# Optimization experiments

Measured on AMD Instinct MI355X. Metric: run time of the kernel, lower is better.

Reference implementation:

```python
import jax, jax.numpy as jnp
import numpy as np

KNN = 16


def _knn_idx(k, ref_xyz, query_xyz):
    # squared euclidean distances: (B, Nq, Nr)
    q2 = jnp.sum(query_xyz * query_xyz, axis=-1, keepdims=True)        # (B, Nq, 1)
    r2 = jnp.sum(ref_xyz * ref_xyz, axis=-1)[:, None, :]               # (B, 1, Nr)
    cross = jnp.einsum('bqc,brc->bqr', query_xyz, ref_xyz)             # (B, Nq, Nr)
    dist = q2 + r2 - 2.0 * cross
    neg_vals, idx = jax.lax.top_k(-dist, k)                            # k smallest dists
    return -neg_vals, idx


def setup_inputs() -> dict:
    key = jax.random.key(0)
    k1, k2, k3, k4 = jax.random.split(key, 4)
    B, N_prev, N_cur, C = 1, 8192, 4096, 256
    return {
        'xyz_prev': jax.random.normal(k1, (B, N_prev, 3), dtype=jnp.float32),
        'xyz_cur': jax.random.normal(k2, (B, N_cur, 3), dtype=jnp.float32),
        'feat_prev': jax.random.normal(k3, (B, N_prev, C), dtype=jnp.float32),
        'feat_cur': jax.random.normal(k4, (B, N_cur, C), dtype=jnp.float32),
    }


def reference(xyz_prev, xyz_cur, feat_prev, feat_cur):
    k = KNN
    _, idx = _knn_idx(k, xyz_prev, xyz_cur)                 # (B, Nq, k) per-batch-local indices
    B, Nq, _ = idx.shape
    C = feat_prev.shape[-1]
    idx_flat = idx.reshape(-1, k).astype(jnp.int32)          # (B*Nq, k)
    prev_flat = feat_prev.reshape(-1, C)                     # (B*Nprev, C)
    cur_flat = feat_cur.reshape(-1, C)                       # (B*Nq, C)
    # faithful to original: gather from flattened table with local indices (batch_dims=0)
    prev_sel = prev_flat[idx_flat]                           # (B*Nq, k, C)
    cur_sel = jnp.broadcast_to(cur_flat[:, None, :], (B * Nq, k, C))
    inter = jnp.concatenate([prev_sel - cur_sel, cur_sel], axis=-1)  # (B*Nq, k, 2C)
    return inter.reshape(B, Nq * k, 2 * C)
```

## Files before the change

kernel.cpp:

```cpp
#include <hip/hip_runtime.h>
#include <stdint.h>

#define KNN 16

typedef float vfloat4 __attribute__((ext_vector_type(4)));

__device__ __forceinline__ uint32_t fkey(float f) {
    uint32_t u = __float_as_uint(f);
    return (u & 0x80000000u) ? ~u : (u | 0x80000000u);
}

__device__ __forceinline__ float inv_fkey_hi(unsigned long long key) {
    const uint32_t k = (uint32_t)(key >> 32);
    if (k == 0xFFFFFFFFu) return __builtin_inff();
    const uint32_t u = (k & 0x80000000u) ? (k ^ 0x80000000u) : ~k;
    return __uint_as_float(u);
}

__device__ __forceinline__ unsigned long long bcast64(unsigned long long x, int l) {
    const uint32_t lo = (uint32_t)__builtin_amdgcn_readlane((int)(uint32_t)x, l);
    const uint32_t hi = (uint32_t)__builtin_amdgcn_readlane((int)(uint32_t)(x >> 32), l);
    return ((unsigned long long)hi << 32) | lo;
}

__device__ __forceinline__ unsigned long long shup1_64(unsigned long long x) {
    const uint32_t lo = (uint32_t)__builtin_amdgcn_update_dpp(
        0, (int)(uint32_t)x, 0x111, 0xF, 0xF, true);
    const uint32_t hi = (uint32_t)__builtin_amdgcn_update_dpp(
        0, (int)(uint32_t)(x >> 32), 0x111, 0xF, 0xF, true);
    return ((unsigned long long)hi << 32) | lo;
}

__global__ __launch_bounds__(256) void prep_kernel(
    const float* __restrict__ xyz_prev, vfloat4* __restrict__ P, int n_prev)
{
    const int i = blockIdx.x * 256 + threadIdx.x;
    if (i >= n_prev) return;
    const float x = xyz_prev[3 * i + 0];
    const float y = xyz_prev[3 * i + 1];
    const float z = xyz_prev[3 * i + 2];
    const float r2 = __fadd_rn(__fadd_rn(__fmul_rn(x, x), __fmul_rn(y, y)),
                               __fmul_rn(z, z));
    vfloat4 v = {x, y, z, r2};
    P[i] = v;
}

__global__ __launch_bounds__(256, 8) void knn_kernel(
    const vfloat4* __restrict__ P, const float* __restrict__ xyz_cur,
    int* __restrict__ knn_idx, int n_prev, int n_cur)
{
    __shared__ unsigned long long smem[2][2][KNN];
    const int lane = threadIdx.x & 63;
    const int qq   = threadIdx.x >> 7;
    const int h    = (threadIdx.x >> 6) & 1;
    const int q    = blockIdx.x * 2 + qq;
    const bool active = q < n_cur;

    if (active) {
        const float qx = xyz_cur[3 * q + 0];
        const float qy = xyz_cur[3 * q + 1];
        const float qz = xyz_cur[3 * q + 2];
        const float q2 = __fadd_rn(__fadd_rn(__fmul_rn(qx, qx), __fmul_rn(qy, qy)),
                                   __fmul_rn(qz, qz));

        const int half_len = ((n_prev + 127) >> 7) << 6;
        const int base = h * half_len;
        const int end  = min((h + 1) * half_len, n_prev);
        const int cnt  = (end > base) ? (end - base) : 0;

        unsigned long long v;
        {
            const int r = base + lane;
            const vfloat4 p = P[r < n_prev ? r : 0];
            const float cr = __fmaf_rn(p.z, qz, __fmaf_rn(p.y, qy, __fmul_rn(p.x, qx)));
            const float dist = __fsub_rn(__fadd_rn(q2, p.w), __fmul_rn(2.0f, cr));
            v = (r < end)
                ? (((unsigned long long)fkey(dist) << 32) | (uint32_t)r)
                : ~0ull;
        }
#pragma unroll
        for (int k = 2; k <= 64; k <<= 1) {
#pragma unroll
            for (int j = k >> 1; j > 0; j >>= 1) {
                const unsigned long long o = __shfl_xor(v, j, 64);
                const bool keepMin = (((lane & k) == 0) == ((lane & j) == 0));
                const bool omin = o < v;
                v = (keepMin == omin) ? o : v;
            }
        }
        unsigned long long lkey = (lane < KNN) ? v : ~0ull;
        unsigned long long tau = bcast64(lkey, 15);
        float tauf = inv_fkey_hi(tau);

        const int n_full = cnt >> 6;
        int t = 1;
        for (; t + 3 < n_full; t += 4) {
            vfloat4 pv[4];
#pragma unroll
            for (int u = 0; u < 4; ++u)
                pv[u] = P[base + ((t + u) << 6) + lane];
#pragma unroll
            for (int u = 0; u < 4; ++u) {
                const int rbase = base + ((t + u) << 6);
                const vfloat4 p = pv[u];
                const float cr = __fmaf_rn(p.z, qz, __fmaf_rn(p.y, qy, __fmul_rn(p.x, qx)));
                const float dist = __fsub_rn(__fadd_rn(q2, p.w), __fmul_rn(2.0f, cr));
                unsigned long long mask = __ballot(dist < tauf);
                while (mask) {
                    const int b = (int)__builtin_ctzll(mask);
                    mask &= mask - 1;
                    const float bd = __uint_as_float(
                        (uint32_t)__builtin_amdgcn_readlane((int)__float_as_uint(dist), b));
                    const unsigned long long bk =
                        (((unsigned long long)fkey(bd)) << 32) | (uint32_t)(rbase + b);
                    if (bk < tau) {
                        const unsigned long long sh = shup1_64(lkey);
                        unsigned long long nk;
                        if (lkey < bk) nk = lkey;
                        else nk = (lane == 0 || sh < bk) ? bk : sh;
                        tau = bcast64(nk, 15);
                        tauf = inv_fkey_hi(tau);
                        if (lane < KNN) lkey = nk;
                    }
                }
            }
        }
        for (; t < n_full; ++t) {
            const int rbase = base + (t << 6);
            const vfloat4 p = P[rbase + lane];
            const float cr = __fmaf_rn(p.z, qz, __fmaf_rn(p.y, qy, __fmul_rn(p.x, qx)));
            const float dist = __fsub_rn(__fadd_rn(q2, p.w), __fmul_rn(2.0f, cr));
            unsigned long long mask = __ballot(dist < tauf);
            while (mask) {
                const int b = (int)__builtin_ctzll(mask);
                mask &= mask - 1;
                const float bd = __uint_as_float(
                    (uint32_t)__builtin_amdgcn_readlane((int)__float_as_uint(dist), b));
                const unsigned long long bk =
                    (((unsigned long long)fkey(bd)) << 32) | (uint32_t)(rbase + b);
                if (bk < tau) {
                    const unsigned long long sh = shup1_64(lkey);
                    unsigned long long nk;
                    if (lkey < bk) nk = lkey;
                    else nk = (lane == 0 || sh < bk) ? bk : sh;
                    tau = bcast64(nk, 15);
                    tauf = inv_fkey_hi(tau);
                    if (lane < KNN) lkey = nk;
                }
            }
        }
        if (n_full >= 1 && (cnt & 63)) {
            const int rbase = base + (n_full << 6);
            const int r = rbase + lane;
            const vfloat4 p = P[r < n_prev ? r : 0];
            const float cr = __fmaf_rn(p.z, qz, __fmaf_rn(p.y, qy, __fmul_rn(p.x, qx)));
            float dist = __fsub_rn(__fadd_rn(q2, p.w), __fmul_rn(2.0f, cr));
            if (r >= end) dist = __builtin_inff();
            unsigned long long mask = __ballot(dist < tauf);
            while (mask) {
                const int b = (int)__builtin_ctzll(mask);
                mask &= mask - 1;
                const float bd = __uint_as_float(
                    (uint32_t)__builtin_amdgcn_readlane((int)__float_as_uint(dist), b));
                const unsigned long long bk =
                    (((unsigned long long)fkey(bd)) << 32) | (uint32_t)(rbase + b);
                if (bk < tau) {
                    const unsigned long long sh = shup1_64(lkey);
                    unsigned long long nk;
                    if (lkey < bk) nk = lkey;
                    else nk = (lane == 0 || sh < bk) ? bk : sh;
                    tau = bcast64(nk, 15);
                    tauf = inv_fkey_hi(tau);
                    if (lane < KNN) lkey = nk;
                }
            }
        }

        if (lane < KNN) smem[qq][h][lane] = lkey;
    }

    __syncthreads();

    if (active && h == 0) {
        unsigned long long v = ~0ull;
        if (lane < 16)      v = smem[qq][0][lane];
        else if (lane < 32) v = smem[qq][1][31 - lane];
#pragma unroll
        for (int j = 16; j > 0; j >>= 1) {
            const unsigned long long o = __shfl_xor(v, j, 64);
            const bool keepMin = ((lane & j) == 0);
            const bool omin = o < v;
            v = (keepMin == omin) ? o : v;
        }
        if (lane < KNN)
            knn_idx[q * KNN + lane] = (int)(v & 0xffffffffu);
    }
}

__global__ __launch_bounds__(256) void combine_kernel(
    const float* __restrict__ feat_prev, const float* __restrict__ feat_cur,
    const int* __restrict__ knn_idx, float* __restrict__ out,
    int n_cur, int c4)
{
    const int w = blockIdx.x * 4 + (threadIdx.x >> 6);
    const int lane = threadIdx.x & 63;
    const int q = w >> 2;
    const int jg = (w & 3) * 4;
    if (q >= n_cur) return;

    int nb[4];
#pragma unroll
    for (int j = 0; j < 4; ++j)
        nb[j] = knn_idx[q * KNN + jg + j];

    const vfloat4* pbase = (const vfloat4*)feat_prev;
    const vfloat4* crow  = (const vfloat4*)feat_cur + (size_t)q * c4;
    const int c8 = 2 * c4;

    for (int i = lane; i < c4; i += 64) {
        const vfloat4 c = crow[i];
        vfloat4 p[4];
#pragma unroll
        for (int j = 0; j < 4; ++j)
            p[j] = pbase[(size_t)nb[j] * c4 + i];

#pragma unroll
        for (int j = 0; j < 4; ++j) {
            vfloat4* orow = (vfloat4*)out + (size_t)(q * KNN + jg + j) * c8;
            __builtin_nontemporal_store(p[j] - c, orow + i);
            __builtin_nontemporal_store(c, orow + c4 + i);
        }
    }
}

extern "C" void kernel_launch(void* const* d_in, const int* in_sizes, int n_in,
                              void* d_out, int out_size, void* d_ws, size_t ws_size,
                              hipStream_t stream) {
    const float* xyz_prev  = (const float*)d_in[0];
    const float* xyz_cur   = (const float*)d_in[1];
    const float* feat_prev = (const float*)d_in[2];
    const float* feat_cur  = (const float*)d_in[3];
    float* out = (float*)d_out;

    const int n_prev = in_sizes[0] / 3;
    const int n_cur  = in_sizes[1] / 3;
    const int C      = in_sizes[2] / n_prev;

    vfloat4* P = (vfloat4*)d_ws;
    int* knn = (int*)((char*)d_ws + (size_t)n_prev * sizeof(vfloat4));

    prep_kernel<<<(n_prev + 255) / 256, 256, 0, stream>>>(xyz_prev, P, n_prev);

    const int knn_blocks = (n_cur + 1) / 2;
    knn_kernel<<<knn_blocks, 256, 0, stream>>>(P, xyz_cur, knn, n_prev, n_cur);

    const int n_waves = n_cur * 4;
    combine_kernel<<<(n_waves + 3) / 4, 256, 0, stream>>>(feat_prev, feat_cur,
                                                          knn, out, n_cur, C / 4);
}
```

Baseline: 206.3 us.

## Assign one wave per KNN query instead of splitting across two waves

```diff
diff --git a/kernel.cpp b/kernel.cpp
--- a/kernel.cpp
+++ b/kernel.cpp
@@ -49,85 +49,51 @@
     const vfloat4* __restrict__ P, const float* __restrict__ xyz_cur,
     int* __restrict__ knn_idx, int n_prev, int n_cur)
 {
-    __shared__ unsigned long long smem[2][2][KNN];
     const int lane = threadIdx.x & 63;
-    const int qq   = threadIdx.x >> 7;
-    const int h    = (threadIdx.x >> 6) & 1;
-    const int q    = blockIdx.x * 2 + qq;
-    const bool active = q < n_cur;
-
-    if (active) {
-        const float qx = xyz_cur[3 * q + 0];
-        const float qy = xyz_cur[3 * q + 1];
-        const float qz = xyz_cur[3 * q + 2];
-        const float q2 = __fadd_rn(__fadd_rn(__fmul_rn(qx, qx), __fmul_rn(qy, qy)),
-                                   __fmul_rn(qz, qz));
-
-        const int half_len = ((n_prev + 127) >> 7) << 6;
-        const int base = h * half_len;
-        const int end  = min((h + 1) * half_len, n_prev);
-        const int cnt  = (end > base) ? (end - base) : 0;
-
-        unsigned long long v;
-        {
-            const int r = base + lane;
-            const vfloat4 p = P[r < n_prev ? r : 0];
-            const float cr = __fmaf_rn(p.z, qz, __fmaf_rn(p.y, qy, __fmul_rn(p.x, qx)));
-            const float dist = __fsub_rn(__fadd_rn(q2, p.w), __fmul_rn(2.0f, cr));
-            v = (r < end)
-                ? (((unsigned long long)fkey(dist) << 32) | (uint32_t)r)
-                : ~0ull;
-        }
-#pragma unroll
-        for (int k = 2; k <= 64; k <<= 1) {
-#pragma unroll
-            for (int j = k >> 1; j > 0; j >>= 1) {
-                const unsigned long long o = __shfl_xor(v, j, 64);
-                const bool keepMin = (((lane & k) == 0) == ((lane & j) == 0));
-                const bool omin = o < v;
-                v = (keepMin == omin) ? o : v;
-            }
-        }
-        unsigned long long lkey = (lane < KNN) ? v : ~0ull;
-        unsigned long long tau = bcast64(lkey, 15);
-        float tauf = inv_fkey_hi(tau);
-
-        const int n_full = cnt >> 6;
-        int t = 1;
-        for (; t + 3 < n_full; t += 4) {
-            vfloat4 pv[4];
-#pragma unroll
-            for (int u = 0; u < 4; ++u)
-                pv[u] = P[base + ((t + u) << 6) + lane];
-#pragma unroll
-            for (int u = 0; u < 4; ++u) {
-                const int rbase = base + ((t + u) << 6);
-                const vfloat4 p = pv[u];
-                const float cr = __fmaf_rn(p.z, qz, __fmaf_rn(p.y, qy, __fmul_rn(p.x, qx)));
-                const float dist = __fsub_rn(__fadd_rn(q2, p.w), __fmul_rn(2.0f, cr));
-                unsigned long long mask = __ballot(dist < tauf);
-                while (mask) {
-                    const int b = (int)__builtin_ctzll(mask);
-                    mask &= mask - 1;
-                    const float bd = __uint_as_float(
-                        (uint32_t)__builtin_amdgcn_readlane((int)__float_as_uint(dist), b));
-                    const unsigned long long bk =
-                        (((unsigned long long)fkey(bd)) << 32) | (uint32_t)(rbase + b);
-                    if (bk < tau) {
-                        const unsigned long long sh = shup1_64(lkey);
-                        unsigned long long nk;
-                        if (lkey < bk) nk = lkey;
-                        else nk = (lane == 0 || sh < bk) ? bk : sh;
-                        tau = bcast64(nk, 15);
-                        tauf = inv_fkey_hi(tau);
-                        if (lane < KNN) lkey = nk;
-                    }
-                }
-            }
-        }
-        for (; t < n_full; ++t) {
-            const int rbase = base + (t << 6);
-            const vfloat4 p = P[rbase + lane];
+    const int q = blockIdx.x * 4 + (threadIdx.x >> 6);
+    if (q >= n_cur) return;
+
+    const float qx = xyz_cur[3 * q + 0];
+    const float qy = xyz_cur[3 * q + 1];
+    const float qz = xyz_cur[3 * q + 2];
+    const float q2 = __fadd_rn(__fadd_rn(__fmul_rn(qx, qx), __fmul_rn(qy, qy)),
+                               __fmul_rn(qz, qz));
+
+    unsigned long long v;
+    {
+        const int r = lane;
+        const vfloat4 p = P[r < n_prev ? r : 0];
+        const float cr = __fmaf_rn(p.z, qz, __fmaf_rn(p.y, qy, __fmul_rn(p.x, qx)));
+        const float dist = __fsub_rn(__fadd_rn(q2, p.w), __fmul_rn(2.0f, cr));
+        v = (r < n_prev)
+            ? (((unsigned long long)fkey(dist) << 32) | (uint32_t)r)
+            : ~0ull;
+    }
+#pragma unroll
+    for (int k = 2; k <= 64; k <<= 1) {
+#pragma unroll
+        for (int j = k >> 1; j > 0; j >>= 1) {
+            const unsigned long long o = __shfl_xor(v, j, 64);
+            const bool keepMin = (((lane & k) == 0) == ((lane & j) == 0));
+            const bool omin = o < v;
+            v = (keepMin == omin) ? o : v;
+        }
+    }
+    unsigned long long lkey = (lane < KNN) ? v : ~0ull;
+    unsigned long long tau = bcast64(lkey, 15);
+    float tauf = inv_fkey_hi(tau);
+
+    const int n_full = n_prev >> 6;
+    int t = 1;
+    for (; t + 3 < n_full; t += 4) {
+        vfloat4 pv[4];
+#pragma unroll
+        for (int u = 0; u < 4; ++u)
+            pv[u] = P[((t + u) << 6) + lane];
+#pragma unroll
+        for (int u = 0; u < 4; ++u) {
+            const int rbase = (t + u) << 6;
+            const vfloat4 p = pv[u];
             const float cr = __fmaf_rn(p.z, qz, __fmaf_rn(p.y, qy, __fmul_rn(p.x, qx)));
             const float dist = __fsub_rn(__fadd_rn(q2, p.w), __fmul_rn(2.0f, cr));
             unsigned long long mask = __ballot(dist < tauf);
@@ -149,52 +115,60 @@
                 }
             }
         }
-        if (n_full >= 1 && (cnt & 63)) {
-            const int rbase = base + (n_full << 6);
-            const int r = rbase + lane;
-            const vfloat4 p = P[r < n_prev ? r : 0];
-            const float cr = __fmaf_rn(p.z, qz, __fmaf_rn(p.y, qy, __fmul_rn(p.x, qx)));
-            float dist = __fsub_rn(__fadd_rn(q2, p.w), __fmul_rn(2.0f, cr));
-            if (r >= end) dist = __builtin_inff();
-            unsigned long long mask = __ballot(dist < tauf);
-            while (mask) {
-                const int b = (int)__builtin_ctzll(mask);
-                mask &= mask - 1;
-                const float bd = __uint_as_float(
-                    (uint32_t)__builtin_amdgcn_readlane((int)__float_as_uint(dist), b));
-                const unsigned long long bk =
-                    (((unsigned long long)fkey(bd)) << 32) | (uint32_t)(rbase + b);
-                if (bk < tau) {
-                    const unsigned long long sh = shup1_64(lkey);
-                    unsigned long long nk;
-                    if (lkey < bk) nk = lkey;
-                    else nk = (lane == 0 || sh < bk) ? bk : sh;
-                    tau = bcast64(nk, 15);
-                    tauf = inv_fkey_hi(tau);
-                    if (lane < KNN) lkey = nk;
-                }
+    }
+    for (; t < n_full; ++t) {
+        const int rbase = t << 6;
+        const vfloat4 p = P[rbase + lane];
+        const float cr = __fmaf_rn(p.z, qz, __fmaf_rn(p.y, qy, __fmul_rn(p.x, qx)));
+        const float dist = __fsub_rn(__fadd_rn(q2, p.w), __fmul_rn(2.0f, cr));
+        unsigned long long mask = __ballot(dist < tauf);
+        while (mask) {
+            const int b = (int)__builtin_ctzll(mask);
+            mask &= mask - 1;
+            const float bd = __uint_as_float(
+                (uint32_t)__builtin_amdgcn_readlane((int)__float_as_uint(dist), b));
+            const unsigned long long bk =
+                (((unsigned long long)fkey(bd)) << 32) | (uint32_t)(rbase + b);
+            if (bk < tau) {
+                const unsigned long long sh = shup1_64(lkey);
+                unsigned long long nk;
+                if (lkey < bk) nk = lkey;
+                else nk = (lane == 0 || sh < bk) ? bk : sh;
+                tau = bcast64(nk, 15);
+                tauf = inv_fkey_hi(tau);
+                if (lane < KNN) lkey = nk;
             }
         }
-
-        if (lane < KNN) smem[qq][h][lane] = lkey;
-    }
-
-    __syncthreads();
-
-    if (active && h == 0) {
-        unsigned long long v = ~0ull;
-        if (lane < 16)      v = smem[qq][0][lane];
-        else if (lane < 32) v = smem[qq][1][31 - lane];
-#pragma unroll
-        for (int j = 16; j > 0; j >>= 1) {
-            const unsigned long long o = __shfl_xor(v, j, 64);
-            const bool keepMin = ((lane & j) == 0);
-            const bool omin = o < v;
-            v = (keepMin == omin) ? o : v;
-        }
-        if (lane < KNN)
-            knn_idx[q * KNN + lane] = (int)(v & 0xffffffffu);
-    }
+    }
+    if (n_prev & 63) {
+        const int rbase = n_full << 6;
+        const int r = rbase + lane;
+        const vfloat4 p = P[r < n_prev ? r : 0];
+        const float cr = __fmaf_rn(p.z, qz, __fmaf_rn(p.y, qy, __fmul_rn(p.x, qx)));
+        float dist = __fsub_rn(__fadd_rn(q2, p.w), __fmul_rn(2.0f, cr));
+        if (r >= n_prev) dist = __builtin_inff();
+        unsigned long long mask = __ballot(dist < tauf);
+        while (mask) {
+            const int b = (int)__builtin_ctzll(mask);
+            mask &= mask - 1;
+            const float bd = __uint_as_float(
+                (uint32_t)__builtin_amdgcn_readlane((int)__float_as_uint(dist), b));
+            const unsigned long long bk =
+                (((unsigned long long)fkey(bd)) << 32) | (uint32_t)(rbase + b);
+            if (bk < tau) {
+                const unsigned long long sh = shup1_64(lkey);
+                unsigned long long nk;
+                if (lkey < bk) nk = lkey;
+                else nk = (lane == 0 || sh < bk) ? bk : sh;
+                tau = bcast64(nk, 15);
+                tauf = inv_fkey_hi(tau);
+                if (lane < KNN) lkey = nk;
+            }
+        }
+    }
+
+    if (lane < KNN)
+        knn_idx[q * KNN + lane] = (int)(lkey & 0xffffffffu);
 }
 
 __global__ __launch_bounds__(256) void combine_kernel(
@@ -251,7 +225,7 @@
 
     prep_kernel<<<(n_prev + 255) / 256, 256, 0, stream>>>(xyz_prev, P, n_prev);
 
-    const int knn_blocks = (n_cur + 1) / 2;
+    const int knn_blocks = (n_cur + 3) / 4;
     knn_kernel<<<knn_blocks, 256, 0, stream>>>(P, xyz_cur, knn, n_prev, n_cur);
 
     const int n_waves = n_cur * 4;
```

Measured after the change: 199.8 us. 3.2% less time.
